# Performance work log

Hardware: AMD Instinct MI355X
Metric: run time of the kernel (lower is better)

## Reference

```python
import jax, jax.numpy as jnp
import numpy as np

N_NODES = 10000
N_EDGES = 640000
IN_FEATS = 128
OUT_FEATS = 128


def setup_inputs() -> dict:
    key = jax.random.key(0)
    k1, k2, k3, k4, k5 = jax.random.split(key, 5)
    x = jax.random.normal(k1, (N_NODES, IN_FEATS), dtype=jnp.float32)
    src = jax.random.randint(k2, (N_EDGES,), 0, N_NODES, dtype=jnp.int64)
    dst = jax.random.randint(k3, (N_EDGES,), 0, N_NODES, dtype=jnp.int64)
    # nn.Linear(in_feats, out_feats): weight [out, in], bias [out]
    bound = 1.0 / np.sqrt(IN_FEATS)
    W = jax.random.uniform(k4, (OUT_FEATS, IN_FEATS), minval=-bound, maxval=bound, dtype=jnp.float32)
    b = jax.random.uniform(k5, (OUT_FEATS,), minval=-bound, maxval=bound, dtype=jnp.float32)
    return {"x": x, "src": src, "dst": dst, "W": W, "b": b}


def reference(x, src, dst, W, b):
    # DGL GINConv (eps=0, sum aggregator): rst = (1+eps)*x + sum_{j->i} x_j, then Linear
    agg = jax.ops.segment_sum(x[src], dst, num_segments=N_NODES)  # [N, in]
    h = x + agg
    return h @ W.T + b  # [N, out]
```

## Files before the change

### kernel.cpp

```cpp
#include <hip/hip_runtime.h>

#define N_NODES 10000
#define N_EDGES 640000
#define FEATS 128
#define NBKT 625
#define CAPB 2048
#define GSTRIDE 16
#define GEMM_WAVES 1250
#define GEMM_GRID 313
#define P1_BLOCKS 79
#define WCVT_BLOCKS 16
#define CLR_BLOCKS 40

typedef __attribute__((ext_vector_type(8))) short short8;
typedef __attribute__((ext_vector_type(4))) float f32x4;

static __device__ __forceinline__ unsigned short f2bf(float f) {
    unsigned int u = __float_as_uint(f);
    u = (u + 0x7FFFu + ((u >> 16) & 1u)) >> 16;
    return (unsigned short)u;
}
static __device__ __forceinline__ float bf2f(unsigned short h) {
    return __uint_as_float((unsigned int)h << 16);
}

__global__ void prep_kernel(const float* __restrict__ W,
                            unsigned short* __restrict__ wb,
                            int* __restrict__ gcur) {
    int blk = blockIdx.x;
    int tid = threadIdx.x;
    if (blk < WCVT_BLOCKS) {
        int i = blk * 256 + tid;
        float4 v = reinterpret_cast<const float4*>(W)[i];
        ushort4 h;
        h.x = f2bf(v.x); h.y = f2bf(v.y); h.z = f2bf(v.z); h.w = f2bf(v.w);
        reinterpret_cast<ushort4*>(wb)[i] = h;
    } else {
        int i = (blk - WCVT_BLOCKS) * 256 + tid;
        if (i < NBKT * GSTRIDE) gcur[i] = 0;
    }
}

__global__ __launch_bounds__(256) void fused_kernel(const float* __restrict__ x,
                                                    const unsigned short* __restrict__ wb,
                                                    const int* __restrict__ src,
                                                    const int* __restrict__ dst,
                                                    unsigned short* __restrict__ ybf,
                                                    int* __restrict__ gcur,
                                                    int* __restrict__ ebuf) {
    __shared__ int lhist[NBKT];
    __shared__ int sbase[NBKT];
    __shared__ int lcur[NBKT];
    int tid = threadIdx.x;

    if (blockIdx.x < GEMM_GRID) {
        int wave = blockIdx.x * 4 + (tid >> 6);
        if (wave >= GEMM_WAVES) return;
        int lane = tid & 63;
        int mtile = wave >> 1;
        int chalf = (wave & 1) * 64;
        int m0 = mtile * 16;
        int mrow = m0 + (lane & 15);
        int kbase = (lane >> 4) * 8;

        short8 ahi[4], alo[4];
        #pragma unroll
        for (int c = 0; c < 4; ++c) {
            const float* xp = x + mrow * FEATS + c * 32 + kbase;
            float4 v0 = *reinterpret_cast<const float4*>(xp);
            float4 v1 = *reinterpret_cast<const float4*>(xp + 4);
            float f[8] = {v0.x, v0.y, v0.z, v0.w, v1.x, v1.y, v1.z, v1.w};
            #pragma unroll
            for (int j = 0; j < 8; ++j) {
                unsigned short h = f2bf(f[j]);
                ahi[c][j] = (short)h;
                alo[c][j] = (short)f2bf(f[j] - bf2f(h));
            }
        }

        int nr = lane & 15;
        int rbase = m0 + (lane >> 4) * 4;
        f32x4 accs[4] = {{0.f,0.f,0.f,0.f},{0.f,0.f,0.f,0.f},
                         {0.f,0.f,0.f,0.f},{0.f,0.f,0.f,0.f}};
        #pragma unroll
        for (int c = 0; c < 4; ++c) {
            short8 bfr[4];
            #pragma unroll
            for (int t = 0; t < 4; ++t) {
                int n = chalf + t * 16 + nr;
                bfr[t] = *reinterpret_cast<const short8*>(wb + n * FEATS + c * 32 + kbase);
            }
            #pragma unroll
            for (int t = 0; t < 4; ++t)
                accs[t] = __builtin_amdgcn_mfma_f32_16x16x32_bf16(ahi[c], bfr[t], accs[t], 0, 0, 0);
            #pragma unroll
            for (int t = 0; t < 4; ++t)
                accs[t] = __builtin_amdgcn_mfma_f32_16x16x32_bf16(alo[c], bfr[t], accs[t], 0, 0, 0);
        }

        #pragma unroll
        for (int t = 0; t < 4; ++t) {
            int col = chalf + t * 16 + (lane & 15);
            #pragma unroll
            for (int r = 0; r < 4; ++r) {
                ybf[(rbase + r) * FEATS + col] = f2bf(accs[t][r]);
            }
        }
        return;
    }

    int blk = blockIdx.x - GEMM_GRID;
    for (int i = tid; i < NBKT; i += 256) lhist[i] = 0;
    __syncthreads();

    const int4* dst4 = reinterpret_cast<const int4*>(dst);
    const int4* src4 = reinterpret_cast<const int4*>(src);
    int i4base = blk * 2048;

    #pragma unroll
    for (int j = 0; j < 8; ++j) {
        int i4 = i4base + j * 256 + tid;
        if (i4 < N_EDGES / 4) {
            int4 d = dst4[i4];
            atomicAdd(&lhist[d.x >> 4], 1);
            atomicAdd(&lhist[d.y >> 4], 1);
            atomicAdd(&lhist[d.z >> 4], 1);
            atomicAdd(&lhist[d.w >> 4], 1);
        }
    }
    __syncthreads();

    for (int i = tid; i < NBKT; i += 256) {
        int c = lhist[i];
        int base = c ? atomicAdd(&gcur[i * GSTRIDE], c) : 0;
        sbase[i] = i * CAPB + base;
        lcur[i] = 0;
    }
    __syncthreads();

    #pragma unroll
    for (int j = 0; j < 8; ++j) {
        int i4 = i4base + j * 256 + tid;
        if (i4 < N_EDGES / 4) {
            int4 d = dst4[i4];
            int4 s = src4[i4];
            int b0 = d.x >> 4, b1 = d.y >> 4, b2 = d.z >> 4, b3 = d.w >> 4;
            int p0 = atomicAdd(&lcur[b0], 1);
            int p1 = atomicAdd(&lcur[b1], 1);
            int p2 = atomicAdd(&lcur[b2], 1);
            int p3 = atomicAdd(&lcur[b3], 1);
            int a0 = sbase[b0] + p0; if (a0 < (b0 + 1) * CAPB) ebuf[a0] = ((d.x & 15) << 16) | s.x;
            int a1 = sbase[b1] + p1; if (a1 < (b1 + 1) * CAPB) ebuf[a1] = ((d.y & 15) << 16) | s.y;
            int a2 = sbase[b2] + p2; if (a2 < (b2 + 1) * CAPB) ebuf[a2] = ((d.z & 15) << 16) | s.z;
            int a3 = sbase[b3] + p3; if (a3 < (b3 + 1) * CAPB) ebuf[a3] = ((d.w & 15) << 16) | s.w;
        }
    }
}

__global__ __launch_bounds__(1024) void pass2_kernel(const unsigned short* __restrict__ ybf,
                                                     const int* __restrict__ ebuf,
                                                     const int* __restrict__ gcur,
                                                     const float* __restrict__ b,
                                                     float* __restrict__ out) {
    __shared__ int q2[CAPB];
    __shared__ int cnts[16];
    __shared__ int offs[17];
    __shared__ int curs[16];
    int bkt = blockIdx.x;
    int tid = threadIdx.x;

    int cnt = gcur[bkt * GSTRIDE];
    if (cnt > CAPB) cnt = CAPB;
    if (cnt < 0) cnt = 0;
    if (tid < 16) cnts[tid] = 0;
    __syncthreads();

    const int* eb = ebuf + bkt * CAPB;
    for (int i = tid; i < cnt; i += 1024) atomicAdd(&cnts[(eb[i] >> 16) & 15], 1);
    __syncthreads();

    if (tid == 0) {
        int a = 0;
        #pragma unroll
        for (int l = 0; l < 16; ++l) { offs[l] = a; curs[l] = a; a += cnts[l]; }
        offs[16] = a;
    }
    __syncthreads();

    for (int i = tid; i < cnt; i += 1024) {
        int v = eb[i];
        int p = atomicAdd(&curs[(v >> 16) & 15], 1);
        q2[p] = v & 0xFFFF;
    }
    __syncthreads();

    int w = tid >> 6;
    int lane = tid & 63;
    int s0 = offs[w];
    int s1 = offs[w + 1];

    float ax = 0.f, ay = 0.f;
    int i = s0;
    for (; i + 8 <= s1; i += 8) {
        int sA[8];
        #pragma unroll
        for (int j = 0; j < 8; ++j) sA[j] = q2[i + j];
        #pragma unroll
        for (int j = 0; j < 8; ++j) {
            ushort2 v = *reinterpret_cast<const ushort2*>(ybf + sA[j] * FEATS + lane * 2);
            ax += bf2f(v.x); ay += bf2f(v.y);
        }
    }
    for (; i < s1; ++i) {
        int s = q2[i];
        ushort2 v = *reinterpret_cast<const ushort2*>(ybf + s * FEATS + lane * 2);
        ax += bf2f(v.x); ay += bf2f(v.y);
    }

    int node = bkt * 16 + w;
    ushort2 sv = *reinterpret_cast<const ushort2*>(ybf + node * FEATS + lane * 2);
    float2 bs = reinterpret_cast<const float2*>(b)[lane];
    float2 o;
    o.x = ax + bf2f(sv.x) + bs.x;
    o.y = ay + bf2f(sv.y) + bs.y;
    reinterpret_cast<float2*>(out + node * FEATS)[lane] = o;
}

extern "C" void kernel_launch(void* const* d_in, const int* in_sizes, int n_in,
                              void* d_out, int out_size, void* d_ws, size_t ws_size,
                              hipStream_t stream) {
    const float* x   = (const float*)d_in[0];
    const int*   src = (const int*)d_in[1];
    const int*   dst = (const int*)d_in[2];
    const float* W   = (const float*)d_in[3];
    const float* b   = (const float*)d_in[4];
    float* out = (float*)d_out;

    unsigned short* wb  = (unsigned short*)d_ws;
    unsigned short* ybf = wb + FEATS * FEATS;
    int* gcur = (int*)(ybf + N_NODES * FEATS);
    int* ebuf = gcur + NBKT * GSTRIDE;

    prep_kernel<<<WCVT_BLOCKS + CLR_BLOCKS, 256, 0, stream>>>(W, wb, gcur);
    fused_kernel<<<GEMM_GRID + P1_BLOCKS, 256, 0, stream>>>(x, wb, src, dst, ybf, gcur, ebuf);
    pass2_kernel<<<NBKT, 1024, 0, stream>>>(ybf, ebuf, gcur, b, out);
}
```

Measured before the change: 99.18 us.

## Drop split-bf16 GEMM correction and use 16-byte row gathers in aggregation

The GEMM stops splitting x into high and low bf16 parts and issues a single bf16 MFMA per tile, halving MFMA work and conversion cost at the price of lower accuracy in the projected features. The aggregation kernel now has each wave read 4 neighbour rows at once, with each lane loading 8 bf16 values (16 bytes) instead of 2. Partial sums are combined with cross-lane shuffles, and only one quarter of the lanes write the output using float4 stores. This cuts the number of load instructions in the gather but adds shuffle reductions and leaves three quarters of the lanes idle during the final write.

```diff
diff --git a/kernel.cpp b/kernel.cpp
--- a/kernel.cpp
+++ b/kernel.cpp
@@ -63,7 +63,7 @@
         int mrow = m0 + (lane & 15);
         int kbase = (lane >> 4) * 8;
 
-        short8 ahi[4], alo[4];
+        short8 a[4];
         #pragma unroll
         for (int c = 0; c < 4; ++c) {
             const float* xp = x + mrow * FEATS + c * 32 + kbase;
@@ -71,11 +71,7 @@
             float4 v1 = *reinterpret_cast<const float4*>(xp + 4);
             float f[8] = {v0.x, v0.y, v0.z, v0.w, v1.x, v1.y, v1.z, v1.w};
             #pragma unroll
-            for (int j = 0; j < 8; ++j) {
-                unsigned short h = f2bf(f[j]);
-                ahi[c][j] = (short)h;
-                alo[c][j] = (short)f2bf(f[j] - bf2f(h));
-            }
+            for (int j = 0; j < 8; ++j) a[c][j] = (short)f2bf(f[j]);
         }
 
         int nr = lane & 15;
@@ -92,10 +88,7 @@
             }
             #pragma unroll
             for (int t = 0; t < 4; ++t)
-                accs[t] = __builtin_amdgcn_mfma_f32_16x16x32_bf16(ahi[c], bfr[t], accs[t], 0, 0, 0);
-            #pragma unroll
-            for (int t = 0; t < 4; ++t)
-                accs[t] = __builtin_amdgcn_mfma_f32_16x16x32_bf16(alo[c], bfr[t], accs[t], 0, 0, 0);
+                accs[t] = __builtin_amdgcn_mfma_f32_16x16x32_bf16(a[c], bfr[t], accs[t], 0, 0, 0);
         }
 
         #pragma unroll
@@ -196,34 +189,61 @@
 
     int w = tid >> 6;
     int lane = tid & 63;
+    int rg = lane >> 4;
+    int fo = lane & 15;
     int s0 = offs[w];
     int s1 = offs[w + 1];
 
-    float ax = 0.f, ay = 0.f;
+    float acc[8] = {};
     int i = s0;
     for (; i + 8 <= s1; i += 8) {
-        int sA[8];
-        #pragma unroll
-        for (int j = 0; j < 8; ++j) sA[j] = q2[i + j];
+        int r0 = q2[i + rg];
+        int r1 = q2[i + 4 + rg];
+        short8 v0 = *reinterpret_cast<const short8*>(ybf + r0 * FEATS + fo * 8);
+        short8 v1 = *reinterpret_cast<const short8*>(ybf + r1 * FEATS + fo * 8);
         #pragma unroll
         for (int j = 0; j < 8; ++j) {
-            ushort2 v = *reinterpret_cast<const ushort2*>(ybf + sA[j] * FEATS + lane * 2);
-            ax += bf2f(v.x); ay += bf2f(v.y);
-        }
-    }
-    for (; i < s1; ++i) {
-        int s = q2[i];
-        ushort2 v = *reinterpret_cast<const ushort2*>(ybf + s * FEATS + lane * 2);
-        ax += bf2f(v.x); ay += bf2f(v.y);
-    }
-
-    int node = bkt * 16 + w;
-    ushort2 sv = *reinterpret_cast<const ushort2*>(ybf + node * FEATS + lane * 2);
-    float2 bs = reinterpret_cast<const float2*>(b)[lane];
-    float2 o;
-    o.x = ax + bf2f(sv.x) + bs.x;
-    o.y = ay + bf2f(sv.y) + bs.y;
-    reinterpret_cast<float2*>(out + node * FEATS)[lane] = o;
+            acc[j] += bf2f((unsigned short)v0[j]);
+            acc[j] += bf2f((unsigned short)v1[j]);
+        }
+    }
+    for (; i + 4 <= s1; i += 4) {
+        int r = q2[i + rg];
+        short8 v = *reinterpret_cast<const short8*>(ybf + r * FEATS + fo * 8);
+        #pragma unroll
+        for (int j = 0; j < 8; ++j) acc[j] += bf2f((unsigned short)v[j]);
+    }
+    if (i + rg < s1) {
+        int r = q2[i + rg];
+        short8 v = *reinterpret_cast<const short8*>(ybf + r * FEATS + fo * 8);
+        #pragma unroll
+        for (int j = 0; j < 8; ++j) acc[j] += bf2f((unsigned short)v[j]);
+    }
+
+    #pragma unroll
+    for (int j = 0; j < 8; ++j) {
+        acc[j] += __shfl_xor(acc[j], 16, 64);
+        acc[j] += __shfl_xor(acc[j], 32, 64);
+    }
+
+    if (rg == 0) {
+        int node = bkt * 16 + w;
+        short8 sv = *reinterpret_cast<const short8*>(ybf + node * FEATS + fo * 8);
+        float4 b0 = reinterpret_cast<const float4*>(b)[fo * 2];
+        float4 b1 = reinterpret_cast<const float4*>(b)[fo * 2 + 1];
+        float4 o0, o1;
+        o0.x = acc[0] + bf2f((unsigned short)sv[0]) + b0.x;
+        o0.y = acc[1] + bf2f((unsigned short)sv[1]) + b0.y;
+        o0.z = acc[2] + bf2f((unsigned short)sv[2]) + b0.z;
+        o0.w = acc[3] + bf2f((unsigned short)sv[3]) + b0.w;
+        o1.x = acc[4] + bf2f((unsigned short)sv[4]) + b1.x;
+        o1.y = acc[5] + bf2f((unsigned short)sv[5]) + b1.y;
+        o1.z = acc[6] + bf2f((unsigned short)sv[6]) + b1.z;
+        o1.w = acc[7] + bf2f((unsigned short)sv[7]) + b1.w;
+        float4* op = reinterpret_cast<float4*>(out + node * FEATS + fo * 8);
+        op[0] = o0;
+        op[1] = o1;
+    }
 }
 
 extern "C" void kernel_launch(void* const* d_in, const int* in_sizes, int n_in,
```

Measured after the change: 100.2 us. Within noise of the previous version (+1.0%).
